# Optimization experiments

Measured on AMD Instinct MI355X. Metric: run time of the kernel, lower is better.

The kernel has to match this reference:

```python
import jax, jax.numpy as jnp
from jax import lax
import numpy as np

STRIDE = 8  # == slice_width
EMBED_DIM = 512


def setup_inputs() -> dict:
    key = jax.random.key(0)
    k0, k1, k2, k3, k4 = jax.random.split(key, 5)
    B, C, H, W = 64, 1, 32, 8192
    images = jax.random.normal(k0, (B, C, H, W), dtype=jnp.float32)
    u = lambda k, s: jax.random.uniform(k, s, jnp.float32, -0.08, 0.08)
    conv_w = u(k1, (1, 1, 3, 3))            # OIHW, 1->1 channel, 3x3
    conv_b = u(k2, (1,))
    lin_w = u(k3, (H * STRIDE, EMBED_DIM))   # bridge: slice_height*slice_width -> embed_dim
    lin_b = u(k4, (EMBED_DIM,))
    return {"images": images, "conv_w": conv_w, "conv_b": conv_b, "lin_w": lin_w, "lin_b": lin_b}


def reference(images, conv_w, conv_b, lin_w, lin_b):
    B, C, H, W = images.shape
    S = W // STRIDE  # src_len (number of width-slices)
    # Windowing: non-overlapping width slices -> a single reshape/transpose
    # [B, C, H, W] -> [B*S, C, H, stride]
    sl = images.reshape(B, C, H, S, STRIDE).transpose(0, 3, 1, 2, 4)
    pixels = sl.reshape(B * S, C, H, STRIDE)
    # Conv2d(1,1,3x3, padding=1) + ReLU (same spatial shape)
    y = lax.conv_general_dilated(
        pixels, conv_w, window_strides=(1, 1), padding="SAME",
        dimension_numbers=("NCHW", "OIHW", "NCHW"))
    y = jax.nn.relu(y + conv_b[None, :, None, None])
    # Bridge linear on flattened slice pixels
    feats = y.reshape(B * S, H * STRIDE)
    emb = feats @ lin_w + lin_b
    return emb.reshape(B, S, EMBED_DIM)
```

## Files before the change

kernel.cpp:

```cpp
#include <hip/hip_runtime.h>
#include <hip/hip_bf16.h>
#include <stdint.h>

#define HEIGHT 32
#define WIDTH  8192
#define KDIM   256
#define NDIM   512
#define BM     64

typedef float f32x4  __attribute__((ext_vector_type(4)));
typedef float f32x16 __attribute__((ext_vector_type(16)));
typedef short bf16x8 __attribute__((ext_vector_type(8)));

__device__ __forceinline__ ushort f2bf(float x) {
  union { float f; uint32_t u; } un; un.f = x;
  uint32_t u = un.u;
  u += 0x7FFFu + ((u >> 16) & 1u);
  return (ushort)(u >> 16);
}

__global__ void prep_w_kernel(const float* __restrict__ lin_w, ushort* __restrict__ wt) {
  int idx = blockIdx.x * 256 + threadIdx.x;
  int k = idx >> 9;
  int n = idx & 511;
  wt[n * KDIM + k] = f2bf(lin_w[k * NDIM + n]);
}

__global__ __launch_bounds__(512) void fused_kernel(
    const float* __restrict__ images, const float* __restrict__ conv_w,
    const float* __restrict__ conv_b, const ushort* __restrict__ wt,
    const float* __restrict__ lin_b, float* __restrict__ out) {
  __shared__ ushort A[BM * KDIM];

  const int tid = threadIdx.x;
  const int rb  = blockIdx.x;
  const int b   = rb >> 4;
  const int s0  = (rb & 15) * BM;

  float cw[9];
#pragma unroll
  for (int i = 0; i < 9; ++i) cw[i] = conv_w[i];
  const float cb = conv_b[0];

  {
    const int sl = tid & 63;
    const int hg = tid >> 6;
    const int h0 = hg * 4;
    const float* base = images + (size_t)b * HEIGHT * WIDTH + (size_t)(s0 + sl) * 8;

    float r[6][8];
#pragma unroll
    for (int i = 0; i < 6; ++i) {
      const int h = h0 - 1 + i;
      if (h >= 0 && h < HEIGHT) {
        const f32x4* p = reinterpret_cast<const f32x4*>(base + (size_t)h * WIDTH);
        f32x4 lo = p[0], hi = p[1];
#pragma unroll
        for (int w = 0; w < 4; ++w) { r[i][w] = lo[w]; r[i][4 + w] = hi[w]; }
      } else {
#pragma unroll
        for (int w = 0; w < 8; ++w) r[i][w] = 0.f;
      }
    }

#pragma unroll
    for (int oh = 0; oh < 4; ++oh) {
      float y[8];
#pragma unroll
      for (int w = 0; w < 8; ++w) y[w] = cb;
#pragma unroll
      for (int dh = 0; dh < 3; ++dh) {
#pragma unroll
        for (int dw = 0; dw < 3; ++dw) {
          const float c = cw[dh * 3 + dw];
#pragma unroll
          for (int w = 0; w < 8; ++w) {
            const int iw = w + dw - 1;
            if (iw >= 0 && iw < 8) y[w] = fmaf(r[oh + dh][iw], c, y[w]);
          }
        }
      }
      bf16x8 pack;
#pragma unroll
      for (int w = 0; w < 8; ++w) pack[w] = (short)f2bf(fmaxf(y[w], 0.f));
      int byte = sl * 512 + (h0 + oh) * 16;
      byte ^= (sl & 7) << 4;
      *reinterpret_cast<bf16x8*>(reinterpret_cast<char*>(A) + byte) = pack;
    }
  }
  __syncthreads();

  const int lane = tid & 63;
  const int wid  = tid >> 6;
  const int n0   = wid * 64;
  const int la   = lane & 31;
  const int lb   = lane >> 5;

  f32x16 acc[2][2];
#pragma unroll
  for (int mf = 0; mf < 2; ++mf)
#pragma unroll
    for (int nf = 0; nf < 2; ++nf)
#pragma unroll
      for (int i = 0; i < 16; ++i) acc[mf][nf][i] = 0.f;

  const ushort* wbase = wt + (size_t)(n0 + la) * KDIM + lb * 8;

#pragma unroll
  for (int k0 = 0; k0 < 16; ++k0) {
    bf16x8 af[2], bfr[2];
#pragma unroll
    for (int mf = 0; mf < 2; ++mf) {
      const int row = mf * 32 + la;
      int byte = row * 512 + k0 * 32 + lb * 16;
      byte ^= (row & 7) << 4;
      af[mf] = *reinterpret_cast<const bf16x8*>(reinterpret_cast<const char*>(A) + byte);
    }
#pragma unroll
    for (int nf = 0; nf < 2; ++nf)
      bfr[nf] = *reinterpret_cast<const bf16x8*>(wbase + nf * 32 * KDIM + k0 * 16);
#pragma unroll
    for (int mf = 0; mf < 2; ++mf)
#pragma unroll
      for (int nf = 0; nf < 2; ++nf)
        acc[mf][nf] = __builtin_amdgcn_mfma_f32_32x32x16_bf16(af[mf], bfr[nf], acc[mf][nf], 0, 0, 0);
  }

  const size_t row0 = (size_t)rb * BM;
#pragma unroll
  for (int mf = 0; mf < 2; ++mf) {
#pragma unroll
    for (int nf = 0; nf < 2; ++nf) {
      const int col = n0 + nf * 32 + la;
      const float bias = lin_b[col];
#pragma unroll
      for (int reg = 0; reg < 16; ++reg) {
        const int rr = mf * 32 + (reg & 3) + 8 * (reg >> 2) + 4 * lb;
        out[(row0 + rr) * NDIM + col] = acc[mf][nf][reg] + bias;
      }
    }
  }
}

extern "C" void kernel_launch(void* const* d_in, const int* in_sizes, int n_in,
                              void* d_out, int out_size, void* d_ws, size_t ws_size,
                              hipStream_t stream) {
  const float* images = (const float*)d_in[0];
  const float* conv_w = (const float*)d_in[1];
  const float* conv_b = (const float*)d_in[2];
  const float* lin_w  = (const float*)d_in[3];
  const float* lin_b  = (const float*)d_in[4];
  float* out = (float*)d_out;
  ushort* wt = (ushort*)d_ws;

  hipLaunchKernelGGL(prep_w_kernel, dim3(512), dim3(256), 0, stream, lin_w, wt);
  hipLaunchKernelGGL(fused_kernel, dim3(1024), dim3(512), 0, stream,
                     images, conv_w, conv_b, wt, lin_b, out);
}
```

Before: 58.62 us.

## Halve row tile to 32 and retile MFMA for more blocks; transpose weights via LDS

The fused conv+GEMM kernel now processes 32 slice rows per block with 256 threads, and each wave computes a 32x128 output strip. That doubles the grid to 2048 blocks and sets launch bounds for 4 blocks per CU to raise occupancy and overlap. The weight prep kernel now transposes through an LDS tile with vectorized loads and stores instead of strided scalar writes, and output stores use nontemporal hints. The cost is that each block loads the full weight matrix for half as many rows, so weight traffic through cache doubles.

```diff
diff --git a/kernel.cpp b/kernel.cpp
--- a/kernel.cpp
+++ b/kernel.cpp
@@ -6,7 +6,7 @@
 #define WIDTH  8192
 #define KDIM   256
 #define NDIM   512
-#define BM     64
+#define BM     32
 
 typedef float f32x4  __attribute__((ext_vector_type(4)));
 typedef float f32x16 __attribute__((ext_vector_type(16)));
@@ -19,14 +19,38 @@
   return (ushort)(u >> 16);
 }
 
-__global__ void prep_w_kernel(const float* __restrict__ lin_w, ushort* __restrict__ wt) {
-  int idx = blockIdx.x * 256 + threadIdx.x;
-  int k = idx >> 9;
-  int n = idx & 511;
-  wt[n * KDIM + k] = f2bf(lin_w[k * NDIM + n]);
+__global__ __launch_bounds__(256) void prep_w_kernel(const float* __restrict__ lin_w,
+                                                     ushort* __restrict__ wt) {
+  __shared__ float T[64][65];
+  const int k0 = (blockIdx.x & 3) * 64;
+  const int n0 = (blockIdx.x >> 2) * 64;
+  {
+    const int kk = threadIdx.x >> 2;
+    const int nq = threadIdx.x & 3;
+    const float* src = lin_w + (size_t)(k0 + kk) * NDIM + n0 + nq * 16;
+#pragma unroll
+    for (int j = 0; j < 4; ++j) {
+      f32x4 v = *reinterpret_cast<const f32x4*>(src + j * 4);
+#pragma unroll
+      for (int e = 0; e < 4; ++e) T[kk][nq * 16 + j * 4 + e] = v[e];
+    }
+  }
+  __syncthreads();
+  {
+    const int nn = threadIdx.x >> 2;
+    const int kq = threadIdx.x & 3;
+    ushort* dst = wt + (size_t)(n0 + nn) * KDIM + k0 + kq * 16;
+    bf16x8 p0, p1;
+#pragma unroll
+    for (int j = 0; j < 8; ++j) p0[j] = (short)f2bf(T[kq * 16 + j][nn]);
+#pragma unroll
+    for (int j = 0; j < 8; ++j) p1[j] = (short)f2bf(T[kq * 16 + 8 + j][nn]);
+    *reinterpret_cast<bf16x8*>(dst) = p0;
+    *reinterpret_cast<bf16x8*>(dst + 8) = p1;
+  }
 }
 
-__global__ __launch_bounds__(512) void fused_kernel(
+__global__ __launch_bounds__(256, 4) void fused_kernel(
     const float* __restrict__ images, const float* __restrict__ conv_w,
     const float* __restrict__ conv_b, const ushort* __restrict__ wt,
     const float* __restrict__ lin_b, float* __restrict__ out) {
@@ -34,8 +58,8 @@
 
   const int tid = threadIdx.x;
   const int rb  = blockIdx.x;
-  const int b   = rb >> 4;
-  const int s0  = (rb & 15) * BM;
+  const int b   = rb >> 5;
+  const int s0  = (rb & 31) * BM;
 
   float cw[9];
 #pragma unroll
@@ -43,8 +67,8 @@
   const float cb = conv_b[0];
 
   {
-    const int sl = tid & 63;
-    const int hg = tid >> 6;
+    const int sl = tid & 31;
+    const int hg = tid >> 5;
     const int h0 = hg * 4;
     const float* base = images + (size_t)b * HEIGHT * WIDTH + (size_t)(s0 + sl) * 8;
 
@@ -92,52 +116,41 @@
 
   const int lane = tid & 63;
   const int wid  = tid >> 6;
-  const int n0   = wid * 64;
+  const int n0   = wid * 128;
   const int la   = lane & 31;
   const int lb   = lane >> 5;
 
-  f32x16 acc[2][2];
+  f32x16 acc[4];
 #pragma unroll
-  for (int mf = 0; mf < 2; ++mf)
+  for (int nf = 0; nf < 4; ++nf)
 #pragma unroll
-    for (int nf = 0; nf < 2; ++nf)
-#pragma unroll
-      for (int i = 0; i < 16; ++i) acc[mf][nf][i] = 0.f;
+    for (int i = 0; i < 16; ++i) acc[nf][i] = 0.f;
 
   const ushort* wbase = wt + (size_t)(n0 + la) * KDIM + lb * 8;
 
 #pragma unroll
   for (int k0 = 0; k0 < 16; ++k0) {
-    bf16x8 af[2], bfr[2];
+    int byte = la * 512 + k0 * 32 + lb * 16;
+    byte ^= (la & 7) << 4;
+    const bf16x8 af = *reinterpret_cast<const bf16x8*>(reinterpret_cast<const char*>(A) + byte);
+    bf16x8 bfr[4];
 #pragma unroll
-    for (int mf = 0; mf < 2; ++mf) {
-      const int row = mf * 32 + la;
-      int byte = row * 512 + k0 * 32 + lb * 16;
-      byte ^= (row & 7) << 4;
-      af[mf] = *reinterpret_cast<const bf16x8*>(reinterpret_cast<const char*>(A) + byte);
-    }
+    for (int nf = 0; nf < 4; ++nf)
+      bfr[nf] = *reinterpret_cast<const bf16x8*>(wbase + (size_t)nf * 32 * KDIM + k0 * 16);
 #pragma unroll
-    for (int nf = 0; nf < 2; ++nf)
-      bfr[nf] = *reinterpret_cast<const bf16x8*>(wbase + nf * 32 * KDIM + k0 * 16);
-#pragma unroll
-    for (int mf = 0; mf < 2; ++mf)
-#pragma unroll
-      for (int nf = 0; nf < 2; ++nf)
-        acc[mf][nf] = __builtin_amdgcn_mfma_f32_32x32x16_bf16(af[mf], bfr[nf], acc[mf][nf], 0, 0, 0);
+    for (int nf = 0; nf < 4; ++nf)
+      acc[nf] = __builtin_amdgcn_mfma_f32_32x32x16_bf16(af, bfr[nf], acc[nf], 0, 0, 0);
   }
 
   const size_t row0 = (size_t)rb * BM;
 #pragma unroll
-  for (int mf = 0; mf < 2; ++mf) {
+  for (int nf = 0; nf < 4; ++nf) {
+    const int col = n0 + nf * 32 + la;
+    const float bias = lin_b[col];
 #pragma unroll
-    for (int nf = 0; nf < 2; ++nf) {
-      const int col = n0 + nf * 32 + la;
-      const float bias = lin_b[col];
-#pragma unroll
-      for (int reg = 0; reg < 16; ++reg) {
-        const int rr = mf * 32 + (reg & 3) + 8 * (reg >> 2) + 4 * lb;
-        out[(row0 + rr) * NDIM + col] = acc[mf][nf][reg] + bias;
-      }
+    for (int reg = 0; reg < 16; ++reg) {
+      const int rr = (reg & 3) + 8 * (reg >> 2) + 4 * lb;
+      __builtin_nontemporal_store(acc[nf][reg] + bias, &out[(row0 + rr) * NDIM + col]);
     }
   }
 }
@@ -153,7 +166,7 @@
   float* out = (float*)d_out;
   ushort* wt = (ushort*)d_ws;
 
-  hipLaunchKernelGGL(prep_w_kernel, dim3(512), dim3(256), 0, stream, lin_w, wt);
-  hipLaunchKernelGGL(fused_kernel, dim3(1024), dim3(512), 0, stream,
+  hipLaunchKernelGGL(prep_w_kernel, dim3(32), dim3(256), 0, stream, lin_w, wt);
+  hipLaunchKernelGGL(fused_kernel, dim3(2048), dim3(256), 0, stream,
                      images, conv_w, conv_b, wt, lin_b, out);
 }
```

Result: slower. 83.30 us (+42.1%).

## Halve fused kernel block size and tile the weight transpose through LDS

Applied to the files above, without the earlier changes.

The weight prep kernel now transposes 64x64 tiles through padded shared memory, using vectorized reads and 16-byte bf16 writes instead of scattered 2-byte stores. The fused kernel drops from 512 to 256 threads per block. Each thread now computes conv output for 8 rows in two passes, and each wave covers two N-chunks of 256 columns in sequence. This aims to make the prep transpose cheaper and to change occupancy and register usage, at the cost of less parallelism inside each block and more serial work per thread.

```diff
diff --git a/kernel.cpp b/kernel.cpp
--- a/kernel.cpp
+++ b/kernel.cpp
@@ -19,14 +19,38 @@
   return (ushort)(u >> 16);
 }
 
-__global__ void prep_w_kernel(const float* __restrict__ lin_w, ushort* __restrict__ wt) {
-  int idx = blockIdx.x * 256 + threadIdx.x;
-  int k = idx >> 9;
-  int n = idx & 511;
-  wt[n * KDIM + k] = f2bf(lin_w[k * NDIM + n]);
+__global__ __launch_bounds__(256) void prep_w_kernel(const float* __restrict__ lin_w,
+                                                     ushort* __restrict__ wt) {
+  __shared__ float T[64][65];
+  const int k0 = (blockIdx.x & 3) * 64;
+  const int n0 = (blockIdx.x >> 2) * 64;
+  {
+    const int kk = threadIdx.x >> 2;
+    const int nq = threadIdx.x & 3;
+    const float* src = lin_w + (size_t)(k0 + kk) * NDIM + n0 + nq * 16;
+#pragma unroll
+    for (int j = 0; j < 4; ++j) {
+      f32x4 v = *reinterpret_cast<const f32x4*>(src + j * 4);
+#pragma unroll
+      for (int e = 0; e < 4; ++e) T[kk][nq * 16 + j * 4 + e] = v[e];
+    }
+  }
+  __syncthreads();
+  {
+    const int nn = threadIdx.x >> 2;
+    const int kq = threadIdx.x & 3;
+    ushort* dst = wt + (size_t)(n0 + nn) * KDIM + k0 + kq * 16;
+    bf16x8 p0, p1;
+#pragma unroll
+    for (int j = 0; j < 8; ++j) p0[j] = (short)f2bf(T[kq * 16 + j][nn]);
+#pragma unroll
+    for (int j = 0; j < 8; ++j) p1[j] = (short)f2bf(T[kq * 16 + 8 + j][nn]);
+    *reinterpret_cast<bf16x8*>(dst) = p0;
+    *reinterpret_cast<bf16x8*>(dst + 8) = p1;
+  }
 }
 
-__global__ __launch_bounds__(512) void fused_kernel(
+__global__ __launch_bounds__(256) void fused_kernel(
     const float* __restrict__ images, const float* __restrict__ conv_w,
     const float* __restrict__ conv_b, const ushort* __restrict__ wt,
     const float* __restrict__ lin_b, float* __restrict__ out) {
@@ -45,98 +69,106 @@
   {
     const int sl = tid & 63;
     const int hg = tid >> 6;
-    const int h0 = hg * 4;
     const float* base = images + (size_t)b * HEIGHT * WIDTH + (size_t)(s0 + sl) * 8;
 
-    float r[6][8];
 #pragma unroll
-    for (int i = 0; i < 6; ++i) {
-      const int h = h0 - 1 + i;
-      if (h >= 0 && h < HEIGHT) {
-        const f32x4* p = reinterpret_cast<const f32x4*>(base + (size_t)h * WIDTH);
-        f32x4 lo = p[0], hi = p[1];
+    for (int g = 0; g < 2; ++g) {
+      const int h0 = hg * 8 + g * 4;
+
+      float r[6][8];
 #pragma unroll
-        for (int w = 0; w < 4; ++w) { r[i][w] = lo[w]; r[i][4 + w] = hi[w]; }
-      } else {
+      for (int i = 0; i < 6; ++i) {
+        const int h = h0 - 1 + i;
+        if (h >= 0 && h < HEIGHT) {
+          const f32x4* p = reinterpret_cast<const f32x4*>(base + (size_t)h * WIDTH);
+          f32x4 lo = p[0], hi = p[1];
 #pragma unroll
-        for (int w = 0; w < 8; ++w) r[i][w] = 0.f;
+          for (int w = 0; w < 4; ++w) { r[i][w] = lo[w]; r[i][4 + w] = hi[w]; }
+        } else {
+#pragma unroll
+          for (int w = 0; w < 8; ++w) r[i][w] = 0.f;
+        }
       }
-    }
 
 #pragma unroll
-    for (int oh = 0; oh < 4; ++oh) {
-      float y[8];
+      for (int oh = 0; oh < 4; ++oh) {
+        float y[8];
 #pragma unroll
-      for (int w = 0; w < 8; ++w) y[w] = cb;
+        for (int w = 0; w < 8; ++w) y[w] = cb;
 #pragma unroll
-      for (int dh = 0; dh < 3; ++dh) {
+        for (int dh = 0; dh < 3; ++dh) {
 #pragma unroll
-        for (int dw = 0; dw < 3; ++dw) {
-          const float c = cw[dh * 3 + dw];
+          for (int dw = 0; dw < 3; ++dw) {
+            const float c = cw[dh * 3 + dw];
 #pragma unroll
-          for (int w = 0; w < 8; ++w) {
-            const int iw = w + dw - 1;
-            if (iw >= 0 && iw < 8) y[w] = fmaf(r[oh + dh][iw], c, y[w]);
+            for (int w = 0; w < 8; ++w) {
+              const int iw = w + dw - 1;
+              if (iw >= 0 && iw < 8) y[w] = fmaf(r[oh + dh][iw], c, y[w]);
+            }
           }
         }
+        bf16x8 pack;
+#pragma unroll
+        for (int w = 0; w < 8; ++w) pack[w] = (short)f2bf(fmaxf(y[w], 0.f));
+        int byte = sl * 512 + (h0 + oh) * 16;
+        byte ^= (sl & 7) << 4;
+        *reinterpret_cast<bf16x8*>(reinterpret_cast<char*>(A) + byte) = pack;
       }
-      bf16x8 pack;
-#pragma unroll
-      for (int w = 0; w < 8; ++w) pack[w] = (short)f2bf(fmaxf(y[w], 0.f));
-      int byte = sl * 512 + (h0 + oh) * 16;
-      byte ^= (sl & 7) << 4;
-      *reinterpret_cast<bf16x8*>(reinterpret_cast<char*>(A) + byte) = pack;
     }
   }
   __syncthreads();
 
   const int lane = tid & 63;
   const int wid  = tid >> 6;
-  const int n0   = wid * 64;
   const int la   = lane & 31;
   const int lb   = lane >> 5;
-
-  f32x16 acc[2][2];
-#pragma unroll
-  for (int mf = 0; mf < 2; ++mf)
-#pragma unroll
-    for (int nf = 0; nf < 2; ++nf)
-#pragma unroll
-      for (int i = 0; i < 16; ++i) acc[mf][nf][i] = 0.f;
-
-  const ushort* wbase = wt + (size_t)(n0 + la) * KDIM + lb * 8;
+  const size_t row0 = (size_t)rb * BM;
 
 #pragma unroll
-  for (int k0 = 0; k0 < 16; ++k0) {
-    bf16x8 af[2], bfr[2];
-#pragma unroll
-    for (int mf = 0; mf < 2; ++mf) {
-      const int row = mf * 32 + la;
-      int byte = row * 512 + k0 * 32 + lb * 16;
-      byte ^= (row & 7) << 4;
-      af[mf] = *reinterpret_cast<const bf16x8*>(reinterpret_cast<const char*>(A) + byte);
-    }
-#pragma unroll
-    for (int nf = 0; nf < 2; ++nf)
-      bfr[nf] = *reinterpret_cast<const bf16x8*>(wbase + nf * 32 * KDIM + k0 * 16);
+  for (int p = 0; p < 2; ++p) {
+    const int n0 = p * 256 + wid * 64;
+
+    f32x16 acc[2][2];
 #pragma unroll
     for (int mf = 0; mf < 2; ++mf)
 #pragma unroll
       for (int nf = 0; nf < 2; ++nf)
-        acc[mf][nf] = __builtin_amdgcn_mfma_f32_32x32x16_bf16(af[mf], bfr[nf], acc[mf][nf], 0, 0, 0);
-  }
+#pragma unroll
+        for (int i = 0; i < 16; ++i) acc[mf][nf][i] = 0.f;
 
-  const size_t row0 = (size_t)rb * BM;
+    const ushort* wbase = wt + (size_t)(n0 + la) * KDIM + lb * 8;
+
 #pragma unroll
-  for (int mf = 0; mf < 2; ++mf) {
+    for (int k0 = 0; k0 < 16; ++k0) {
+      bf16x8 af[2], bfr[2];
 #pragma unroll
-    for (int nf = 0; nf < 2; ++nf) {
-      const int col = n0 + nf * 32 + la;
-      const float bias = lin_b[col];
+      for (int mf = 0; mf < 2; ++mf) {
+        const int row = mf * 32 + la;
+        int byte = row * 512 + k0 * 32 + lb * 16;
+        byte ^= (row & 7) << 4;
+        af[mf] = *reinterpret_cast<const bf16x8*>(reinterpret_cast<const char*>(A) + byte);
+      }
 #pragma unroll
-      for (int reg = 0; reg < 16; ++reg) {
-        const int rr = mf * 32 + (reg & 3) + 8 * (reg >> 2) + 4 * lb;
-        out[(row0 + rr) * NDIM + col] = acc[mf][nf][reg] + bias;
+      for (int nf = 0; nf < 2; ++nf)
+        bfr[nf] = *reinterpret_cast<const bf16x8*>(wbase + (size_t)nf * 32 * KDIM + k0 * 16);
+#pragma unroll
+      for (int mf = 0; mf < 2; ++mf)
+#pragma unroll
+        for (int nf = 0; nf < 2; ++nf)
+          acc[mf][nf] = __builtin_amdgcn_mfma_f32_32x32x16_bf16(af[mf], bfr[nf], acc[mf][nf], 0, 0, 0);
+    }
+
+#pragma unroll
+    for (int mf = 0; mf < 2; ++mf) {
+#pragma unroll
+      for (int nf = 0; nf < 2; ++nf) {
+        const int col = n0 + nf * 32 + la;
+        const float bias = lin_b[col];
+#pragma unroll
+        for (int reg = 0; reg < 16; ++reg) {
+          const int rr = mf * 32 + (reg & 3) + 8 * (reg >> 2) + 4 * lb;
+          out[(row0 + rr) * NDIM + col] = acc[mf][nf][reg] + bias;
+        }
       }
     }
   }
@@ -153,7 +185,7 @@
   float* out = (float*)d_out;
   ushort* wt = (ushort*)d_ws;
 
-  hipLaunchKernelGGL(prep_w_kernel, dim3(512), dim3(256), 0, stream, lin_w, wt);
-  hipLaunchKernelGGL(fused_kernel, dim3(1024), dim3(512), 0, stream,
+  hipLaunchKernelGGL(prep_w_kernel, dim3(32), dim3(256), 0, stream, lin_w, wt);
+  hipLaunchKernelGGL(fused_kernel, dim3(1024), dim3(256), 0, stream,
                      images, conv_w, conv_b, wt, lin_b, out);
 }
```

After: 61.81 us. 1.05x slower.

## Split fused conv+GEMM into separate conv and GEMM kernels via workspace

Applied to the files above, without the earlier changes.

When the workspace is large enough, a conv kernel writes bf16 features for all slices to global memory, and a separate GEMM kernel reads them back. The weight transpose and bf16 conversion is folded into extra blocks of the conv kernel to save one launch. Each GEMM wave computes a 32-row tile across all 512 output columns. This adds a 32 MB round trip to global memory for the intermediate features in exchange for simpler kernels that may achieve higher occupancy. If the workspace is too small, the code falls back to the original fused path.

```diff
diff --git a/kernel.cpp b/kernel.cpp
--- a/kernel.cpp
+++ b/kernel.cpp
@@ -6,7 +6,9 @@
 #define WIDTH  8192
 #define KDIM   256
 #define NDIM   512
-#define BM     64
+#define NSLICES 65536
+#define WT_BYTES (NDIM * KDIM * 2)
+#define FEATS_BYTES ((size_t)NSLICES * KDIM * 2)
 
 typedef float f32x4  __attribute__((ext_vector_type(4)));
 typedef float f32x16 __attribute__((ext_vector_type(16)));
@@ -19,13 +21,141 @@
   return (ushort)(u >> 16);
 }
 
-__global__ void prep_w_kernel(const float* __restrict__ lin_w, ushort* __restrict__ wt) {
-  int idx = blockIdx.x * 256 + threadIdx.x;
-  int k = idx >> 9;
-  int n = idx & 511;
-  wt[n * KDIM + k] = f2bf(lin_w[k * NDIM + n]);
-}
-
+__device__ __forceinline__ void load_row8(float* r, const float* p) {
+  f32x4 lo = *reinterpret_cast<const f32x4*>(p);
+  f32x4 hi = *reinterpret_cast<const f32x4*>(p + 4);
+#pragma unroll
+  for (int w = 0; w < 4; ++w) { r[w] = lo[w]; r[4 + w] = hi[w]; }
+}
+
+__device__ __forceinline__ void prep_wt_body(const float* __restrict__ lin_w,
+                                             ushort* __restrict__ wt, int bid, int tid) {
+  const int base = bid * 2048 + tid * 8;
+#pragma unroll
+  for (int j = 0; j < 8; ++j) {
+    const int idx = base + j;
+    const int n = idx >> 8, k = idx & 255;
+    wt[n * KDIM + k] = f2bf(lin_w[(size_t)k * NDIM + n]);
+  }
+}
+
+__global__ __launch_bounds__(256) void prep_wt_kernel(const float* __restrict__ lin_w,
+                                                      ushort* __restrict__ wt) {
+  prep_wt_body(lin_w, wt, blockIdx.x, threadIdx.x);
+}
+
+__global__ __launch_bounds__(256) void conv_kernel(
+    const float* __restrict__ images, const float* __restrict__ conv_w,
+    const float* __restrict__ conv_b, const float* __restrict__ lin_w,
+    ushort* __restrict__ wt, ushort* __restrict__ feats) {
+  const int blk = blockIdx.x;
+  const int tid = threadIdx.x;
+  if (blk >= 512) { prep_wt_body(lin_w, wt, blk - 512, tid); return; }
+
+  float cw[9];
+#pragma unroll
+  for (int i = 0; i < 9; ++i) cw[i] = conv_w[i];
+  const float cb = conv_b[0];
+
+  const int sl = tid & 127;
+  const int hf = tid >> 7;
+  const int s  = blk * 128 + sl;
+  const int b  = s >> 10;
+  const int slb = s & 1023;
+  const float* base = images + (size_t)b * (HEIGHT * WIDTH) + (size_t)slb * 8;
+  ushort* fo = feats + (size_t)s * KDIM;
+  const int h0 = hf * 16;
+
+  float pr[8], cu[8], nx[8];
+  if (h0 > 0) load_row8(pr, base + (size_t)(h0 - 1) * WIDTH);
+  else {
+#pragma unroll
+    for (int w = 0; w < 8; ++w) pr[w] = 0.f;
+  }
+  load_row8(cu, base + (size_t)h0 * WIDTH);
+
+#pragma unroll
+  for (int i = 0; i < 16; ++i) {
+    const int h = h0 + i;
+    if (h + 1 < HEIGHT) load_row8(nx, base + (size_t)(h + 1) * WIDTH);
+    else {
+#pragma unroll
+      for (int w = 0; w < 8; ++w) nx[w] = 0.f;
+    }
+    float y[8];
+#pragma unroll
+    for (int w = 0; w < 8; ++w) y[w] = cb;
+#pragma unroll
+    for (int dw = 0; dw < 3; ++dw) {
+      const float c0 = cw[dw], c1 = cw[3 + dw], c2 = cw[6 + dw];
+#pragma unroll
+      for (int w = 0; w < 8; ++w) {
+        const int iw = w + dw - 1;
+        if (iw >= 0 && iw < 8) {
+          y[w] = fmaf(pr[iw], c0, y[w]);
+          y[w] = fmaf(cu[iw], c1, y[w]);
+          y[w] = fmaf(nx[iw], c2, y[w]);
+        }
+      }
+    }
+    bf16x8 pack;
+#pragma unroll
+    for (int w = 0; w < 8; ++w) pack[w] = (short)f2bf(fmaxf(y[w], 0.f));
+    *reinterpret_cast<bf16x8*>(fo + h * 8) = pack;
+#pragma unroll
+    for (int w = 0; w < 8; ++w) { pr[w] = cu[w]; cu[w] = nx[w]; }
+  }
+}
+
+__global__ __launch_bounds__(256) void gemm_kernel(
+    const ushort* __restrict__ feats, const ushort* __restrict__ wt,
+    const float* __restrict__ lin_b, float* __restrict__ out) {
+  const int tid  = threadIdx.x;
+  const int lane = tid & 63;
+  const int wv   = tid >> 6;
+  const int mtile = blockIdx.x * 4 + wv;
+  const int la = lane & 31;
+  const int lb = lane >> 5;
+
+  const ushort* arow = feats + (size_t)mtile * 32 * KDIM + (size_t)la * KDIM + lb * 8;
+  const size_t row0 = (size_t)mtile * 32;
+
+  for (int p = 0; p < 4; ++p) {
+    const int n0 = p * 128;
+    f32x16 acc[4];
+#pragma unroll
+    for (int nf = 0; nf < 4; ++nf)
+#pragma unroll
+      for (int i = 0; i < 16; ++i) acc[nf][i] = 0.f;
+
+    const ushort* wb = wt + (size_t)(n0 + la) * KDIM + lb * 8;
+
+#pragma unroll
+    for (int k0 = 0; k0 < 16; ++k0) {
+      const bf16x8 af = *reinterpret_cast<const bf16x8*>(arow + k0 * 16);
+      bf16x8 bfr[4];
+#pragma unroll
+      for (int nf = 0; nf < 4; ++nf)
+        bfr[nf] = *reinterpret_cast<const bf16x8*>(wb + (size_t)nf * 32 * KDIM + k0 * 16);
+#pragma unroll
+      for (int nf = 0; nf < 4; ++nf)
+        acc[nf] = __builtin_amdgcn_mfma_f32_32x32x16_bf16(af, bfr[nf], acc[nf], 0, 0, 0);
+    }
+
+#pragma unroll
+    for (int nf = 0; nf < 4; ++nf) {
+      const int col = n0 + nf * 32 + la;
+      const float bias = lin_b[col];
+#pragma unroll
+      for (int reg = 0; reg < 16; ++reg) {
+        const int rr = (reg & 3) + 8 * (reg >> 2) + 4 * lb;
+        out[(row0 + rr) * NDIM + col] = acc[nf][reg] + bias;
+      }
+    }
+  }
+}
+
+#define BM 64
 __global__ __launch_bounds__(512) void fused_kernel(
     const float* __restrict__ images, const float* __restrict__ conv_w,
     const float* __restrict__ conv_b, const ushort* __restrict__ wt,
@@ -52,12 +182,8 @@
 #pragma unroll
     for (int i = 0; i < 6; ++i) {
       const int h = h0 - 1 + i;
-      if (h >= 0 && h < HEIGHT) {
-        const f32x4* p = reinterpret_cast<const f32x4*>(base + (size_t)h * WIDTH);
-        f32x4 lo = p[0], hi = p[1];
-#pragma unroll
-        for (int w = 0; w < 4; ++w) { r[i][w] = lo[w]; r[i][4 + w] = hi[w]; }
-      } else {
+      if (h >= 0 && h < HEIGHT) load_row8(r[i], base + (size_t)h * WIDTH);
+      else {
 #pragma unroll
         for (int w = 0; w < 8; ++w) r[i][w] = 0.f;
       }
@@ -118,7 +244,7 @@
     }
 #pragma unroll
     for (int nf = 0; nf < 2; ++nf)
-      bfr[nf] = *reinterpret_cast<const bf16x8*>(wbase + nf * 32 * KDIM + k0 * 16);
+      bfr[nf] = *reinterpret_cast<const bf16x8*>(wbase + (size_t)nf * 32 * KDIM + k0 * 16);
 #pragma unroll
     for (int mf = 0; mf < 2; ++mf)
 #pragma unroll
@@ -153,7 +279,15 @@
   float* out = (float*)d_out;
   ushort* wt = (ushort*)d_ws;
 
-  hipLaunchKernelGGL(prep_w_kernel, dim3(512), dim3(256), 0, stream, lin_w, wt);
-  hipLaunchKernelGGL(fused_kernel, dim3(1024), dim3(512), 0, stream,
-                     images, conv_w, conv_b, wt, lin_b, out);
-}
+  if (ws_size >= (size_t)WT_BYTES + FEATS_BYTES) {
+    ushort* feats = (ushort*)((char*)d_ws + WT_BYTES);
+    hipLaunchKernelGGL(conv_kernel, dim3(576), dim3(256), 0, stream,
+                       images, conv_w, conv_b, lin_w, wt, feats);
+    hipLaunchKernelGGL(gemm_kernel, dim3(512), dim3(256), 0, stream,
+                       feats, wt, lin_b, out);
+  } else {
+    hipLaunchKernelGGL(prep_wt_kernel, dim3(64), dim3(256), 0, stream, lin_w, wt);
+    hipLaunchKernelGGL(fused_kernel, dim3(1024), dim3(512), 0, stream,
+                       images, conv_w, conv_b, wt, lin_b, out);
+  }
+}
```

New measurement: 114.6 us. +95.5%, slower.
